# Optimization experiments

Measured on AMD Instinct MI355X. Metric: run time of the kernel, lower is better.

## Reference

```python
import jax, jax.numpy as jnp
import numpy as np

B, N, D, H = 2, 2048, 1024, 16
HD = D // H  # 64
EPS = 1e-6


def setup_inputs() -> dict:
    key = jax.random.key(0)
    ks = jax.random.split(key, 16)
    rnd = lambda k, shp: jax.random.normal(k, shp, dtype=jnp.float32)
    w = lambda k, i, o: rnd(k, (i, o)) * 0.02  # stored as (in, out); y = x @ W
    return {
        "x": rnd(ks[0], (B, N, D)),
        "emb_B_D": rnd(ks[1], (B, D)),
        "gate": rnd(ks[2], (B, D)),
        "crossattn_emb": rnd(ks[3], (B, 128, D)),
        "rope_emb_L_1_1_D": rnd(ks[4], (N, HD)),
        "Wq1": w(ks[5], D, D), "Wq2": w(ks[6], D, D),
        "Wk1": w(ks[7], D, D), "Wk2": w(ks[8], D, D),
        "Wv": w(ks[9], D, D),
        "Wo": w(ks[10], D, D),
        "Wada1": w(ks[11], D, D),
        "Wada2": w(ks[12], D, 2 * D),
        "bada2": jnp.zeros((2 * D,), dtype=jnp.float32),
    }


def rotate_half(t):
    t1, t2 = jnp.split(t, 2, axis=-1)
    return jnp.concatenate([-t2, t1], axis=-1)


def reference(x, emb_B_D, gate, crossattn_emb, rope_emb_L_1_1_D,
              Wq1, Wq2, Wk1, Wk2, Wv, Wo, Wada1, Wada2, bada2):
    # adaLN modulation: SiLU -> Linear(no bias) -> Linear(bias)
    ada = jax.nn.silu(emb_B_D) @ Wada1 @ Wada2 + bada2          # [B, 2D]
    shift, scale = jnp.split(ada, 2, axis=1)                    # [B, D] each

    # LayerNorm (no affine) + scale/shift
    mu = jnp.mean(x, axis=-1, keepdims=True)
    var = jnp.var(x, axis=-1, keepdims=True)
    xn = (x - mu) * jax.lax.rsqrt(var + EPS)
    xn = xn * (1.0 + scale[:, None, :]) + shift[:, None, :]     # [B, N, D]

    # QKV projections (each to_q/to_k is two stacked linears, to_v one)
    q = xn @ Wq1 @ Wq2
    k = xn @ Wk1 @ Wk2
    v = xn @ Wv
    split_heads = lambda t: t.reshape(B, N, H, HD).transpose(0, 2, 1, 3)  # b h n d
    q, k, v = split_heads(q), split_heads(k), split_heads(v)

    # RoPE
    cos = jnp.cos(rope_emb_L_1_1_D)[None, None]                 # [1,1,N,HD]
    sin = jnp.sin(rope_emb_L_1_1_D)[None, None]
    q = q * cos + rotate_half(q) * sin
    k = k * cos + rotate_half(k) * sin

    # Attention
    sim = jnp.einsum("bhid,bhjd->bhij", q, k) * (HD ** -0.5)
    attn = jax.nn.softmax(sim, axis=-1)
    out = jnp.einsum("bhij,bhjd->bhid", attn, v)
    out = out.transpose(0, 2, 1, 3).reshape(B, N, D) @ Wo

    # Gated residual
    return x + gate[:, None, :] * out
```

## Files before the change

kernel.cpp:

```cpp
#include <hip/hip_runtime.h>
#include <stdint.h>
#include <math.h>

typedef unsigned short u16;
typedef __attribute__((ext_vector_type(8))) short short8;
typedef __attribute__((ext_vector_type(4))) float f32x4;
typedef __attribute__((ext_vector_type(4))) unsigned short u16x4;
typedef __attribute__((ext_vector_type(2))) unsigned int uint2v;

#define DEV static __device__ __forceinline__

DEV u16 f2bf(float f) {
    unsigned u = __builtin_bit_cast(unsigned, f);
    u = u + 0x7fffu + ((u >> 16) & 1u);
    return (u16)(u >> 16);
}
DEV float bf2f(u16 s) { return __builtin_bit_cast(float, ((unsigned)s) << 16); }
DEV unsigned pk2(float a, float b) {
    unsigned ua = __builtin_bit_cast(unsigned, a) + 0x8000u;
    unsigned ub = __builtin_bit_cast(unsigned, b) + 0x8000u;
    return (ua >> 16) | (ub & 0xffff0000u);
}

DEV void gl_lds16(const u16* g, u16* l) {
#if __has_builtin(__builtin_amdgcn_global_load_lds)
    __builtin_amdgcn_global_load_lds((const __attribute__((address_space(1))) unsigned int*)g,
                                     (__attribute__((address_space(3))) unsigned int*)l, 16, 0, 0);
#else
    *(short8*)l = *(const short8*)g;
#endif
}


__global__ __launch_bounds__(256) void k_ada1(const float* __restrict__ emb, const float* __restrict__ W,
                                              float* __restrict__ out) {
    int col = blockIdx.x * 64 + (threadIdx.x & 63);
    int b = blockIdx.y;
    int kseg = threadIdx.x >> 6;
    float acc = 0.f;
    for (int k = kseg * 256; k < kseg * 256 + 256; k++) {
        float e = emb[b * 1024 + k];
        float se = e / (1.f + __expf(-e));
        acc += se * W[(size_t)k * 1024 + col];
    }
    __shared__ float red[4][64];
    red[kseg][threadIdx.x & 63] = acc;
    __syncthreads();
    if (threadIdx.x < 64)
        out[b * 1024 + blockIdx.x * 64 + threadIdx.x] =
            red[0][threadIdx.x] + red[1][threadIdx.x] + red[2][threadIdx.x] + red[3][threadIdx.x];
}

__global__ __launch_bounds__(256) void k_ada2(const float* __restrict__ t, const float* __restrict__ W,
                                              const float* __restrict__ bias, float* __restrict__ out) {
    int col = blockIdx.x * 64 + (threadIdx.x & 63);
    int b = blockIdx.y;
    int kseg = threadIdx.x >> 6;
    float acc = 0.f;
    for (int k = kseg * 256; k < kseg * 256 + 256; k++)
        acc += t[b * 1024 + k] * W[(size_t)k * 2048 + col];
    __shared__ float red[4][64];
    red[kseg][threadIdx.x & 63] = acc;
    __syncthreads();
    if (threadIdx.x < 64) {
        int c = blockIdx.x * 64 + threadIdx.x;
        out[b * 2048 + c] = red[0][threadIdx.x] + red[1][threadIdx.x] +
                            red[2][threadIdx.x] + red[3][threadIdx.x] + bias[c];
    }
}

__global__ __launch_bounds__(256) void k_conv(const float* s0, u16* d0, const float* s1, u16* d1,
                                              const float* s2, u16* d2, const float* s3, u16* d3,
                                              const float* s4, u16* d4, const float* s5, u16* d5) {
    __shared__ u16 tile[64][65];
    const float* s; u16* d;
    switch (blockIdx.z) {
        case 0: s = s0; d = d0; break;
        case 1: s = s1; d = d1; break;
        case 2: s = s2; d = d2; break;
        case 3: s = s3; d = d3; break;
        case 4: s = s4; d = d4; break;
        default: s = s5; d = d5; break;
    }
    int k0 = blockIdx.x * 64, n0 = blockIdx.y * 64;
    int tx = threadIdx.x & 63, ty = threadIdx.x >> 6;
    if (blockIdx.z >= 4) {
        #pragma unroll
        for (int i = 0; i < 16; i++) {
            int kk = ty + 4 * i;
            d[(size_t)(k0 + kk) * 1024 + n0 + tx] = f2bf(s[(size_t)(k0 + kk) * 1024 + n0 + tx]);
        }
        return;
    }
    #pragma unroll
    for (int i = 0; i < 16; i++) {
        int kk = ty + 4 * i;
        tile[kk][tx] = f2bf(s[(size_t)(k0 + kk) * 1024 + n0 + tx]);
    }
    __syncthreads();
    #pragma unroll
    for (int i = 0; i < 16; i++) {
        int nn = ty + 4 * i;
        d[(size_t)(n0 + nn) * 1024 + k0 + tx] = tile[tx][nn];
    }
}

__global__ __launch_bounds__(256) void k_ln(const float* __restrict__ x, const float* __restrict__ ada,
                                            u16* __restrict__ xn, const float* __restrict__ rope,
                                            float* __restrict__ cst, float* __restrict__ snt) {
    if (blockIdx.x < 512) {
        int idx = blockIdx.x * 256 + threadIdx.x;
        float sv, cv;
        __sincosf(rope[idx], &sv, &cv);
        cst[idx] = cv; snt[idx] = sv;
    }
    int row = blockIdx.x;
    int b = row >> 11;
    float4 v = ((const float4*)(x + (size_t)row * 1024))[threadIdx.x];
    float s = v.x + v.y + v.z + v.w;
    float ss = v.x * v.x + v.y * v.y + v.z * v.z + v.w * v.w;
    #pragma unroll
    for (int m = 1; m < 64; m <<= 1) { s += __shfl_xor(s, m, 64); ss += __shfl_xor(ss, m, 64); }
    __shared__ float red[2][4];
    int wave = threadIdx.x >> 6, lane = threadIdx.x & 63;
    if (lane == 0) { red[0][wave] = s; red[1][wave] = ss; }
    __syncthreads();
    s = red[0][0] + red[0][1] + red[0][2] + red[0][3];
    ss = red[1][0] + red[1][1] + red[1][2] + red[1][3];
    float mu = s * (1.f / 1024.f);
    float var = ss * (1.f / 1024.f) - mu * mu;
    float rs = rsqrtf(var + 1e-6f);
    int c = threadIdx.x * 4;
    const float* sh = ada + b * 2048;
    const float* sc = ada + b * 2048 + 1024;
    u16x4 r;
    r.x = f2bf((v.x - mu) * rs * (1.f + sc[c + 0]) + sh[c + 0]);
    r.y = f2bf((v.y - mu) * rs * (1.f + sc[c + 1]) + sh[c + 1]);
    r.z = f2bf((v.z - mu) * rs * (1.f + sc[c + 2]) + sh[c + 2]);
    r.w = f2bf((v.w - mu) * rs * (1.f + sc[c + 3]) + sh[c + 3]);
    *(u16x4*)(xn + (size_t)row * 1024 + c) = r;
}

template <int BM, int BN, int MODE>
DEV void gemm_core(const u16* __restrict__ A, const u16* __restrict__ Bt,
                   u16* __restrict__ Cb, float* __restrict__ Cf,
                   const float* __restrict__ Xres, const float* __restrict__ gate,
                   const float* __restrict__ cst, const float* __restrict__ snt,
                   float scale, int Nn, int K, int m0, int n0) {
    constexpr int MI = BM / 32, NJ = BN / 32;
    __shared__ u16 As[BM][64];
    __shared__ u16 Bs[BN][64];
    int tid = threadIdx.x;
    int lane = tid & 63, wave = tid >> 6;
    int wm = (wave & 1) * (BM / 2), wn = (wave >> 1) * (BN / 2);
    int lr = lane & 15, quad = lane >> 4;
    f32x4 acc[MI][NJ];
    #pragma unroll
    for (int i = 0; i < MI; i++)
        #pragma unroll
        for (int j = 0; j < NJ; j++) acc[i][j] = f32x4{0.f, 0.f, 0.f, 0.f};

    int arow = tid >> 3;
    int acol = (tid & 7) * 8;
    int g8 = (((tid & 7) ^ (arow & 7))) * 8;
    int cc[2] = { ((quad ^ (lr & 7))) * 8, (((4 + quad) ^ (lr & 7))) * 8 };

    for (int k0 = 0; k0 < K; k0 += 64) {
        #pragma unroll
        for (int p = 0; p < MI; p++)
            gl_lds16(A + (size_t)(m0 + arow + 32 * p) * K + k0 + g8, &As[arow + 32 * p][acol]);
        #pragma unroll
        for (int p = 0; p < NJ; p++)
            gl_lds16(Bt + (size_t)(n0 + arow + 32 * p) * K + k0 + g8, &Bs[arow + 32 * p][acol]);
        __syncthreads();
        #pragma unroll
        for (int ks = 0; ks < 2; ks++) {
            short8 af[MI], bfr[NJ];
            #pragma unroll
            for (int i = 0; i < MI; i++) af[i] = *(const short8*)(&As[wm + i * 16 + lr][cc[ks]]);
            #pragma unroll
            for (int j = 0; j < NJ; j++) bfr[j] = *(const short8*)(&Bs[wn + j * 16 + lr][cc[ks]]);
            #pragma unroll
            for (int i = 0; i < MI; i++)
                #pragma unroll
                for (int j = 0; j < NJ; j++)
                    acc[i][j] = __builtin_amdgcn_mfma_f32_16x16x32_bf16(af[i], bfr[j], acc[i][j], 0, 0, 0);
        }
        __syncthreads();
    }

    if (MODE == 2 && (n0 + wn) < 2048) {
        #pragma unroll
        for (int i = 0; i < MI; i++)
            #pragma unroll
            for (int jp = 0; jp < 2; jp++)
                #pragma unroll
                for (int r = 0; r < 4; r++) {
                    int row = m0 + wm + i * 16 + quad * 4 + r;
                    int n = row & 2047;
                    int d1 = jp * 16 + lr;
                    float c1 = cst[n * 64 + d1],      s1 = snt[n * 64 + d1];
                    float c2 = cst[n * 64 + d1 + 32], s2 = snt[n * 64 + d1 + 32];
                    float x1 = acc[i][jp][r], x2 = acc[i][jp + 2][r];
                    Cb[(size_t)row * Nn + n0 + wn + d1]      = f2bf(x1 * c1 - x2 * s1);
                    Cb[(size_t)row * Nn + n0 + wn + d1 + 32] = f2bf(x2 * c2 + x1 * s2);
                }
        return;
    }
    #pragma unroll
    for (int i = 0; i < MI; i++)
        #pragma unroll
        for (int j = 0; j < NJ; j++)
            #pragma unroll
            for (int r = 0; r < 4; r++) {
                int row = m0 + wm + i * 16 + quad * 4 + r;
                int col = n0 + wn + j * 16 + lr;
                float v = acc[i][j][r];
                if (MODE == 1) {
                    int b = row >> 11;
                    Cf[(size_t)row * Nn + col] = Xres[(size_t)row * Nn + col] + gate[b * 1024 + col] * v;
                } else {
                    Cb[(size_t)row * Nn + col] = f2bf(v * scale);
                }
            }
}

template <int BM, int BN, int MODE>
__global__ __launch_bounds__(256) void gemm_bt(const u16* __restrict__ A, const u16* __restrict__ Bt,
                                               u16* __restrict__ Cb, float* __restrict__ Cf,
                                               const float* __restrict__ Xres, const float* __restrict__ gate,
                                               const float* __restrict__ cst, const float* __restrict__ snt,
                                               int Nn, int K) {
    gemm_core<BM, BN, MODE>(A, Bt, Cb, Cf, Xres, gate, cst, snt, 1.f, Nn, K,
                            blockIdx.y * BM, blockIdx.x * BN);
}

__global__ __launch_bounds__(256) void gemm_fold(const u16* A0, const u16* B0, u16* C0,
                                                 const u16* A1, const u16* B1, u16* C1) {
    const u16* A = blockIdx.z ? A1 : A0;
    const u16* Bt = blockIdx.z ? B1 : B0;
    u16* C = blockIdx.z ? C1 : C0;
    float scale = blockIdx.z ? 1.0f : 0.125f;
    gemm_core<64, 64, 0>(A, Bt, C, nullptr, nullptr, nullptr, nullptr, nullptr, scale,
                         1024, 1024, blockIdx.y * 64, blockIdx.x * 64);
}

__global__ __launch_bounds__(256) void k_vtrans(const u16* __restrict__ v, u16* __restrict__ vt) {
    __shared__ u16 tile[64][65];
    int n0 = blockIdx.x * 64;
    int bh = blockIdx.y; int b = bh >> 4, h = bh & 15;
    int tx = threadIdx.x & 63, ty = threadIdx.x >> 6;
    #pragma unroll
    for (int i = 0; i < 16; i++) {
        int nn = ty + 4 * i;
        tile[nn][tx] = v[(size_t)(b * 2048 + n0 + nn) * 3072 + 2048 + h * 64 + tx];
    }
    __syncthreads();
    #pragma unroll
    for (int i = 0; i < 16; i++) {
        int dd = ty + 4 * i;
        vt[((size_t)bh * 64 + dd) * 2048 + n0 + tx] = tile[tx][dd];
    }
}

__global__ __launch_bounds__(256) void k_attn(const u16* __restrict__ qkv, const u16* __restrict__ vt,
                                              u16* __restrict__ ob) {
    __shared__ u16 pool[128 * 72];
    __shared__ u16 Ks[2][64][64];
    __shared__ u16 Vs[2][64][64];
    int q0 = blockIdx.x * 128;
    int bh = blockIdx.y; int b = bh >> 4, h = bh & 15;
    int tid = threadIdx.x;
    int lane = tid & 63, wave = tid >> 6;
    int lr = lane & 15, quad = lane >> 4;
    int srow = tid >> 3, scol = (tid & 7) * 8;
    int sg = (((tid & 7) ^ (srow & 7))) * 8;
    int cc[2] = { ((quad ^ (lr & 7))) * 8, (((4 + quad) ^ (lr & 7))) * 8 };

    #pragma unroll
    for (int p = 0; p < 4; p++)
        gl_lds16(qkv + ((size_t)(b * 2048 + q0 + srow + 32 * p)) * 3072 + h * 64 + sg,
                 pool + (srow + 32 * p) * 64 + scol);
    #pragma unroll
    for (int p = 0; p < 2; p++) {
        gl_lds16(qkv + ((size_t)(b * 2048 + srow + 32 * p)) * 3072 + 1024 + h * 64 + sg,
                 &Ks[0][srow + 32 * p][scol]);
        gl_lds16(vt + ((size_t)(bh * 64 + srow + 32 * p)) * 2048 + sg,
                 &Vs[0][srow + 32 * p][scol]);
    }
    __syncthreads();
    short8 qf[2][2];
    #pragma unroll
    for (int rt = 0; rt < 2; rt++)
        #pragma unroll
        for (int ks = 0; ks < 2; ks++)
            qf[rt][ks] = *(const short8*)(pool + (wave * 32 + rt * 16 + lr) * 64 + cc[ks]);
    __syncthreads();

    float l_part[2] = {0.f, 0.f};
    f32x4 oacc[2][4];
    #pragma unroll
    for (int rt = 0; rt < 2; rt++)
        #pragma unroll
        for (int dt = 0; dt < 4; dt++) oacc[rt][dt] = f32x4{0.f, 0.f, 0.f, 0.f};

    for (int it = 0; it < 32; ++it) {
        int cur = it & 1, nxt = cur ^ 1;
        if (it < 31) {
            int k0 = (it + 1) * 64;
            #pragma unroll
            for (int p = 0; p < 2; p++) {
                gl_lds16(qkv + ((size_t)(b * 2048 + k0 + srow + 32 * p)) * 3072 + 1024 + h * 64 + sg,
                         &Ks[nxt][srow + 32 * p][scol]);
                gl_lds16(vt + ((size_t)(bh * 64 + srow + 32 * p)) * 2048 + k0 + sg,
                         &Vs[nxt][srow + 32 * p][scol]);
            }
        }
        f32x4 st[2][4];
        #pragma unroll
        for (int rt = 0; rt < 2; rt++)
            #pragma unroll
            for (int ct = 0; ct < 4; ct++) st[rt][ct] = f32x4{0.f, 0.f, 0.f, 0.f};
        #pragma unroll
        for (int ks = 0; ks < 2; ks++) {
            short8 kf[4];
            #pragma unroll
            for (int ct = 0; ct < 4; ct++)
                kf[ct] = *(const short8*)(&Ks[cur][ct * 16 + lr][cc[ks]]);
            #pragma unroll
            for (int rt = 0; rt < 2; rt++)
                #pragma unroll
                for (int ct = 0; ct < 4; ct++)
                    st[rt][ct] = __builtin_amdgcn_mfma_f32_16x16x32_bf16(kf[ct], qf[rt][ks], st[rt][ct], 0, 0, 0);
        }
        #pragma unroll
        for (int rt = 0; rt < 2; rt++)
            #pragma unroll
            for (int ct = 0; ct < 4; ct++) {
                float p0 = __expf(st[rt][ct][0]);
                float p1 = __expf(st[rt][ct][1]);
                float p2 = __expf(st[rt][ct][2]);
                float p3 = __expf(st[rt][ct][3]);
                l_part[rt] += (p0 + p1) + (p2 + p3);
                uint2v w; w.x = pk2(p0, p1); w.y = pk2(p2, p3);
                *(uint2v*)(pool + (wave * 32 + rt * 16 + lr) * 72 + ct * 16 + quad * 4) = w;
            }
        #pragma unroll
        for (int ks = 0; ks < 2; ks++) {
            short8 pf[2], vf[4];
            #pragma unroll
            for (int rt = 0; rt < 2; rt++)
                pf[rt] = *(const short8*)(pool + (wave * 32 + rt * 16 + lr) * 72 + ks * 32 + quad * 8);
            #pragma unroll
            for (int dt = 0; dt < 4; dt++)
                vf[dt] = *(const short8*)(&Vs[cur][dt * 16 + lr][cc[ks]]);
            #pragma unroll
            for (int rt = 0; rt < 2; rt++)
                #pragma unroll
                for (int dt = 0; dt < 4; dt++)
                    oacc[rt][dt] = __builtin_amdgcn_mfma_f32_16x16x32_bf16(pf[rt], vf[dt], oacc[rt][dt], 0, 0, 0);
        }
        __syncthreads();
    }
    float* linv = (float*)&Ks[0][0][0];
    #pragma unroll
    for (int rt = 0; rt < 2; rt++) {
        float l = l_part[rt];
        l += __shfl_xor(l, 16, 64);
        l += __shfl_xor(l, 32, 64);
        if (quad == 0) linv[wave * 32 + rt * 16 + lr] = 1.f / l;
    }
    __syncthreads();
    #pragma unroll
    for (int rt = 0; rt < 2; rt++) {
        float iv[4];
        #pragma unroll
        for (int r = 0; r < 4; r++) iv[r] = linv[wave * 32 + rt * 16 + quad * 4 + r];
        #pragma unroll
        for (int dt = 0; dt < 4; dt++)
            #pragma unroll
            for (int r = 0; r < 4; r++) {
                int row = q0 + wave * 32 + rt * 16 + quad * 4 + r;
                ob[((size_t)(b * 2048 + row)) * 1024 + h * 64 + dt * 16 + lr] = f2bf(oacc[rt][dt][r] * iv[r]);
            }
    }
}

extern "C" void kernel_launch(void* const* d_in, const int* in_sizes, int n_in,
                              void* d_out, int out_size, void* d_ws, size_t ws_size,
                              hipStream_t stream) {
    const float* x     = (const float*)d_in[0];
    const float* emb   = (const float*)d_in[1];
    const float* gate  = (const float*)d_in[2];
    const float* rope  = (const float*)d_in[4];
    const float* Wq1   = (const float*)d_in[5];
    const float* Wq2   = (const float*)d_in[6];
    const float* Wk1   = (const float*)d_in[7];
    const float* Wk2   = (const float*)d_in[8];
    const float* Wv    = (const float*)d_in[9];
    const float* Wo    = (const float*)d_in[10];
    const float* Wada1 = (const float*)d_in[11];
    const float* Wada2 = (const float*)d_in[12];
    const float* bada2 = (const float*)d_in[13];
    float* out = (float*)d_out;

    char* ws = (char*)d_ws;
    size_t off = 0;
    auto alloc = [&](size_t bytes) { void* p = ws + off; off += (bytes + 255) & ~(size_t)255; return p; };
    float* t_ada = (float*)alloc(2048 * 4);
    float* ada   = (float*)alloc(4096 * 4);
    float* cst   = (float*)alloc((size_t)131072 * 4);
    float* snt   = (float*)alloc((size_t)131072 * 4);
    u16* xn    = (u16*)alloc((size_t)4096 * 1024 * 2);
    u16* Wq1b  = (u16*)alloc((size_t)1024 * 1024 * 2);
    u16* Wk1b  = (u16*)alloc((size_t)1024 * 1024 * 2);
    u16* Wq2t  = (u16*)alloc((size_t)1024 * 1024 * 2);
    u16* Wk2t  = (u16*)alloc((size_t)1024 * 1024 * 2);
    u16* Wot   = (u16*)alloc((size_t)1024 * 1024 * 2);
    u16* WqkvT = (u16*)alloc((size_t)3072 * 1024 * 2);
    u16* qkvb  = (u16*)alloc((size_t)4096 * 3072 * 2);
    u16* vtb   = (u16*)alloc((size_t)4096 * 1024 * 2);
    u16* aob   = (u16*)alloc((size_t)4096 * 1024 * 2);
    (void)ws_size; (void)in_sizes; (void)n_in; (void)out_size;

    k_ada1<<<dim3(16, 2), 256, 0, stream>>>(emb, Wada1, t_ada);
    k_ada2<<<dim3(32, 2), 256, 0, stream>>>(t_ada, Wada2, bada2, ada);

    k_conv<<<dim3(16, 16, 6), 256, 0, stream>>>(Wq2, Wq2t, Wk2, Wk2t,
                                                Wv, WqkvT + (size_t)2048 * 1024, Wo, Wot,
                                                Wq1, Wq1b, Wk1, Wk1b);

    k_ln<<<4096, 256, 0, stream>>>(x, ada, xn, rope, cst, snt);

    gemm_fold<<<dim3(16, 16, 2), 256, 0, stream>>>(Wq2t, Wq1b, WqkvT,
                                                   Wk2t, Wk1b, WqkvT + (size_t)1024 * 1024);

    gemm_bt<128, 128, 2><<<dim3(24, 32), 256, 0, stream>>>(xn, WqkvT, qkvb, nullptr, nullptr, nullptr,
                                                           cst, snt, 3072, 1024);

    k_vtrans<<<dim3(32, 32), 256, 0, stream>>>(qkvb, vtb);

    k_attn<<<dim3(16, 32), 256, 0, stream>>>(qkvb, vtb, aob);

    gemm_bt<128, 64, 1><<<dim3(16, 32), 256, 0, stream>>>(aob, Wot, nullptr, out, x, gate,
                                                          nullptr, nullptr, 1024, 1024);
}
```

Baseline: 306.4 us.

## Split attention over two key halves with register-prefetched K/V and combine kernel

The attention kernel now splits the key dimension into two halves using a third grid dimension. This doubles the number of blocks, so more blocks can run on each CU. Each split writes unnormalized fp32 partial outputs and row sums to workspace, and a new combine kernel adds them, normalizes, and writes the bf16 result. K/V tile staging changes from direct global-to-LDS copies to register prefetch two iterations ahead, with LDS stores after compute. The cost is extra fp32 partial traffic to global memory and one more kernel launch.

After: 306.5 us. About the same (+0.0%).

```diff
diff --git a/kernel.cpp b/kernel.cpp
--- a/kernel.cpp
+++ b/kernel.cpp
@@ -264,12 +264,14 @@
 }
 
 __global__ __launch_bounds__(256) void k_attn(const u16* __restrict__ qkv, const u16* __restrict__ vt,
-                                              u16* __restrict__ ob) {
+                                              float* __restrict__ paO, float* __restrict__ paL) {
     __shared__ u16 pool[128 * 72];
     __shared__ u16 Ks[2][64][64];
     __shared__ u16 Vs[2][64][64];
     int q0 = blockIdx.x * 128;
     int bh = blockIdx.y; int b = bh >> 4, h = bh & 15;
+    int z = blockIdx.z;
+    int kbase = z * 1024;
     int tid = threadIdx.x;
     int lane = tid & 63, wave = tid >> 6;
     int lr = lane & 15, quad = lane >> 4;
@@ -277,17 +279,17 @@
     int sg = (((tid & 7) ^ (srow & 7))) * 8;
     int cc[2] = { ((quad ^ (lr & 7))) * 8, (((4 + quad) ^ (lr & 7))) * 8 };
 
+    const u16* kp = qkv + ((size_t)(b * 2048 + kbase + srow)) * 3072 + 1024 + h * 64 + sg;
+    const u16* vp = vt + ((size_t)(bh * 64 + srow)) * 2048 + kbase + sg;
+
     #pragma unroll
     for (int p = 0; p < 4; p++)
         gl_lds16(qkv + ((size_t)(b * 2048 + q0 + srow + 32 * p)) * 3072 + h * 64 + sg,
                  pool + (srow + 32 * p) * 64 + scol);
-    #pragma unroll
-    for (int p = 0; p < 2; p++) {
-        gl_lds16(qkv + ((size_t)(b * 2048 + srow + 32 * p)) * 3072 + 1024 + h * 64 + sg,
-                 &Ks[0][srow + 32 * p][scol]);
-        gl_lds16(vt + ((size_t)(bh * 64 + srow + 32 * p)) * 2048 + sg,
-                 &Vs[0][srow + 32 * p][scol]);
-    }
+
+    short8 krA[2], vrA[2], krB[2], vrB[2];
+    krA[0] = *(const short8*)(kp);               krA[1] = *(const short8*)(kp + (size_t)32 * 3072);
+    vrA[0] = *(const short8*)(vp);               vrA[1] = *(const short8*)(vp + (size_t)32 * 2048);
     __syncthreads();
     short8 qf[2][2];
     #pragma unroll
@@ -295,6 +297,12 @@
         #pragma unroll
         for (int ks = 0; ks < 2; ks++)
             qf[rt][ks] = *(const short8*)(pool + (wave * 32 + rt * 16 + lr) * 64 + cc[ks]);
+    *(short8*)(&Ks[0][srow][scol])      = krA[0];
+    *(short8*)(&Ks[0][srow + 32][scol]) = krA[1];
+    *(short8*)(&Vs[0][srow][scol])      = vrA[0];
+    *(short8*)(&Vs[0][srow + 32][scol]) = vrA[1];
+    krB[0] = *(const short8*)(kp + (size_t)64 * 3072);  krB[1] = *(const short8*)(kp + (size_t)96 * 3072);
+    vrB[0] = *(const short8*)(vp + 64);                 vrB[1] = *(const short8*)(vp + 64 + (size_t)32 * 2048);
     __syncthreads();
 
     float l_part[2] = {0.f, 0.f};
@@ -304,17 +312,13 @@
         #pragma unroll
         for (int dt = 0; dt < 4; dt++) oacc[rt][dt] = f32x4{0.f, 0.f, 0.f, 0.f};
 
-    for (int it = 0; it < 32; ++it) {
-        int cur = it & 1, nxt = cur ^ 1;
-        if (it < 31) {
-            int k0 = (it + 1) * 64;
-            #pragma unroll
-            for (int p = 0; p < 2; p++) {
-                gl_lds16(qkv + ((size_t)(b * 2048 + k0 + srow + 32 * p)) * 3072 + 1024 + h * 64 + sg,
-                         &Ks[nxt][srow + 32 * p][scol]);
-                gl_lds16(vt + ((size_t)(bh * 64 + srow + 32 * p)) * 2048 + k0 + sg,
-                         &Vs[nxt][srow + 32 * p][scol]);
-            }
+    auto body = [&](int it, int cur, short8 (&krF)[2], short8 (&vrF)[2],
+                    short8 (&krH)[2], short8 (&vrH)[2]) {
+        if (it < 14) {
+            const u16* kq = kp + (size_t)(it + 2) * 64 * 3072;
+            const u16* vq = vp + (it + 2) * 64;
+            krF[0] = *(const short8*)(kq);  krF[1] = *(const short8*)(kq + (size_t)32 * 3072);
+            vrF[0] = *(const short8*)(vq);  vrF[1] = *(const short8*)(vq + (size_t)32 * 2048);
         }
         f32x4 st[2][4];
         #pragma unroll
@@ -360,30 +364,59 @@
                 for (int dt = 0; dt < 4; dt++)
                     oacc[rt][dt] = __builtin_amdgcn_mfma_f32_16x16x32_bf16(pf[rt], vf[dt], oacc[rt][dt], 0, 0, 0);
         }
+        if (it < 15) {
+            int nxt = cur ^ 1;
+            *(short8*)(&Ks[nxt][srow][scol])      = krH[0];
+            *(short8*)(&Ks[nxt][srow + 32][scol]) = krH[1];
+            *(short8*)(&Vs[nxt][srow][scol])      = vrH[0];
+            *(short8*)(&Vs[nxt][srow + 32][scol]) = vrH[1];
+        }
         __syncthreads();
-    }
-    float* linv = (float*)&Ks[0][0][0];
+    };
+
+    #pragma unroll 1
+    for (int it2 = 0; it2 < 8; ++it2) {
+        body(2 * it2,     0, krA, vrA, krB, vrB);
+        body(2 * it2 + 1, 1, krB, vrB, krA, vrA);
+    }
+
     #pragma unroll
     for (int rt = 0; rt < 2; rt++) {
         float l = l_part[rt];
         l += __shfl_xor(l, 16, 64);
         l += __shfl_xor(l, 32, 64);
-        if (quad == 0) linv[wave * 32 + rt * 16 + lr] = 1.f / l;
-    }
-    __syncthreads();
-    #pragma unroll
-    for (int rt = 0; rt < 2; rt++) {
-        float iv[4];
-        #pragma unroll
-        for (int r = 0; r < 4; r++) iv[r] = linv[wave * 32 + rt * 16 + quad * 4 + r];
+        if (quad == 0)
+            paL[(size_t)z * 65536 + bh * 2048 + q0 + wave * 32 + rt * 16 + lr] = l;
+    }
+    float* po = paO + (size_t)z * 4096 * 1024;
+    #pragma unroll
+    for (int rt = 0; rt < 2; rt++)
         #pragma unroll
         for (int dt = 0; dt < 4; dt++)
             #pragma unroll
             for (int r = 0; r < 4; r++) {
                 int row = q0 + wave * 32 + rt * 16 + quad * 4 + r;
-                ob[((size_t)(b * 2048 + row)) * 1024 + h * 64 + dt * 16 + lr] = f2bf(oacc[rt][dt][r] * iv[r]);
+                po[((size_t)(b * 2048 + row)) * 1024 + h * 64 + dt * 16 + lr] = oacc[rt][dt][r];
             }
-    }
+}
+
+__global__ __launch_bounds__(256) void k_comb(const float* __restrict__ paO, const float* __restrict__ paL,
+                                              u16* __restrict__ aob) {
+    int row = blockIdx.x;
+    int b = row >> 11, n = row & 2047;
+    int c = threadIdx.x * 4;
+    int h = c >> 6;
+    float l0 = paL[(b * 16 + h) * 2048 + n];
+    float l1 = paL[65536 + (b * 16 + h) * 2048 + n];
+    float inv = 1.f / (l0 + l1);
+    float4 o0 = *(const float4*)(paO + (size_t)row * 1024 + c);
+    float4 o1 = *(const float4*)(paO + (size_t)4096 * 1024 + (size_t)row * 1024 + c);
+    u16x4 r;
+    r.x = f2bf((o0.x + o1.x) * inv);
+    r.y = f2bf((o0.y + o1.y) * inv);
+    r.z = f2bf((o0.z + o1.z) * inv);
+    r.w = f2bf((o0.w + o1.w) * inv);
+    *(u16x4*)(aob + (size_t)row * 1024 + c) = r;
 }
 
 extern "C" void kernel_launch(void* const* d_in, const int* in_sizes, int n_in,
@@ -421,6 +454,8 @@
     u16* qkvb  = (u16*)alloc((size_t)4096 * 3072 * 2);
     u16* vtb   = (u16*)alloc((size_t)4096 * 1024 * 2);
     u16* aob   = (u16*)alloc((size_t)4096 * 1024 * 2);
+    float* paO = (float*)alloc((size_t)2 * 4096 * 1024 * 4);
+    float* paL = (float*)alloc((size_t)2 * 65536 * 4);
     (void)ws_size; (void)in_sizes; (void)n_in; (void)out_size;
 
     k_ada1<<<dim3(16, 2), 256, 0, stream>>>(emb, Wada1, t_ada);
@@ -440,7 +475,8 @@
 
     k_vtrans<<<dim3(32, 32), 256, 0, stream>>>(qkvb, vtb);
 
-    k_attn<<<dim3(16, 32), 256, 0, stream>>>(qkvb, vtb, aob);
+    k_attn<<<dim3(16, 32, 2), 256, 0, stream>>>(qkvb, vtb, paO, paL);
+    k_comb<<<4096, 256, 0, stream>>>(paO, paL, aob);
 
     gemm_bt<128, 64, 1><<<dim3(16, 32), 256, 0, stream>>>(aob, Wot, nullptr, out, x, gate,
                                                           nullptr, nullptr, 1024, 1024);
```
